# Kernel tuning notes

Hardware: AMD Instinct MI355X
Metric: run time of the kernel (lower is better)

## Reference

```python
import jax, jax.numpy as jnp
import numpy as np

BOX = 5  # box_size (odd)
PATTERN_SCALE = 16.0


def setup_inputs() -> dict:
    key = jax.random.key(0)
    k1, k2 = jax.random.split(key)
    x = jax.random.normal(k1, (1, 1, 480, 640), dtype=jnp.float32)
    # buffer: uniform in [-pattern_scale, pattern_scale], shape [num_pairs, 2, 2]
    pair_offsets = (jax.random.uniform(k2, (256, 2, 2), dtype=jnp.float32) - 0.5) * 2.0 * PATTERN_SCALE
    return {"x": x, "pair_offsets": pair_offsets}


def _box_average(x, box):
    # replicate-pad then stride-1 average pool => same-size box average
    pad = box // 2
    xp = jnp.pad(x, ((0, 0), (0, 0), (pad, pad), (pad, pad)), mode='edge')
    s = jax.lax.reduce_window(xp, 0.0, jax.lax.add,
                              (1, 1, box, box), (1, 1, 1, 1), 'VALID')
    return s / float(box * box)


def _grid_sample_offsets(img_flat, offsets, B, H, W):
    """Bilinear grid_sample with border padding, align_corners=True,
    for per-pair translational grids. img_flat: [B, H*W]; offsets: [P, 2] (dy, dx).
    Returns [B, P, H, W]."""
    scale_y = 2.0 / (H - 1 + 1e-8)
    scale_x = 2.0 / (W - 1 + 1e-8)
    base_y = jnp.linspace(-1.0, 1.0, H, dtype=img_flat.dtype)[None, :, None]  # [1,H,1]
    base_x = jnp.linspace(-1.0, 1.0, W, dtype=img_flat.dtype)[None, None, :]  # [1,1,W]
    gy = base_y + offsets[:, 0, None, None] * scale_y  # [P,H,1]
    gx = base_x + offsets[:, 1, None, None] * scale_x  # [P,1,W]
    # unnormalize (align_corners=True) and clip coords (padding_mode='border')
    py = jnp.clip((gy + 1.0) * 0.5 * (H - 1), 0.0, H - 1.0)  # [P,H,1]
    px = jnp.clip((gx + 1.0) * 0.5 * (W - 1), 0.0, W - 1.0)  # [P,1,W]
    y0 = jnp.floor(py)
    x0 = jnp.floor(px)
    wy = py - y0  # [P,H,1]
    wx = px - x0  # [P,1,W]
    y0i = y0.astype(jnp.int32)
    x0i = x0.astype(jnp.int32)
    y1i = jnp.minimum(y0i + 1, H - 1)
    x1i = jnp.minimum(x0i + 1, W - 1)

    def gather(yi, xi):
        idx = yi * W + xi  # broadcast -> [P,H,W]
        return jnp.take(img_flat, idx, axis=1)  # [B,P,H,W]

    v = (gather(y0i, x0i) * (1.0 - wy) * (1.0 - wx)
         + gather(y0i, x1i) * (1.0 - wy) * wx
         + gather(y1i, x0i) * wy * (1.0 - wx)
         + gather(y1i, x1i) * wy * wx)
    return v


def reference(x, pair_offsets):
    B, C, H, W = x.shape
    box_avg = _box_average(x, BOX)            # [B,1,H,W]
    img_flat = box_avg[:, 0].reshape(B, H * W)
    s1 = _grid_sample_offsets(img_flat, pair_offsets[:, 0, :], B, H, W)
    s2 = _grid_sample_offsets(img_flat, pair_offsets[:, 1, :], B, H, W)
    return s1 - s2  # binarize=False -> raw differences, [B, P, H, W]
```

## Files before the change

kernel.cpp:

```cpp
#include <hip/hip_runtime.h>

#define H 480
#define W 640
#define NP 256
#define HW (H * W)

#define P1_BLK 16
#define P2_BLK 9
#define P3_BLK 120

#define P1_TOTAL (NP * P1_BLK)
#define P2_TOTAL (NP * (P1_BLK + P2_BLK))
#define TOTAL_BLK (NP * (P1_BLK + P2_BLK + P3_BLK))

__global__ __launch_bounds__(256) void box_avg_kernel(const float* __restrict__ x,
                                                      float* __restrict__ box) {
    int idx = blockIdx.x * 256 + threadIdx.x;
    int i = idx / W;
    int j = idx - i * W;
    float s = 0.f;
#pragma unroll
    for (int dy = -2; dy <= 2; ++dy) {
        int yy = min(max(i + dy, 0), H - 1);
        const float* row = x + yy * W;
#pragma unroll
        for (int dx = -2; dx <= 2; ++dx) {
            int xx = min(max(j + dx, 0), W - 1);
            s += row[xx];
        }
    }
    box[idx] = s * 0.04f;
}

template<int S>
__device__ __forceinline__ void hlerp8(const float4 P, const float4 Q, const float4 R,
                                       float wx, float h[8]) {
    const float c[12] = {P.x, P.y, P.z, P.w, Q.x, Q.y, Q.z, Q.w, R.x, R.y, R.z, R.w};
#pragma unroll
    for (int k = 0; k < 8; ++k)
        h[k] = fmaf(wx, c[S + k + 1] - c[S + k], c[S + k]);
}

#define DISPATCH_H(sv, ...)                              \
    switch (sv) {                                        \
        case 0:  hlerp8<0>(__VA_ARGS__); break;          \
        case 1:  hlerp8<1>(__VA_ARGS__); break;          \
        case 2:  hlerp8<2>(__VA_ARGS__); break;          \
        default: hlerp8<3>(__VA_ARGS__); break;          \
    }

__global__ __launch_bounds__(256) void bad_desc_kernel(const float* __restrict__ box,
                                                       const float* __restrict__ po,
                                                       float* __restrict__ out) {
    int b = blockIdx.x;
    if (b < P1_TOTAL) {
        int p = b >> 4;
        int t = ((b - (p << 4)) << 8) + threadIdx.x;
        int band = t / 72;
        if (band >= 56) return;
        int g = t - band * 72;
        int i0 = 16 + (band << 3);
        int j  = 32 + (g << 3);

        float dy1 = po[p * 4 + 0];
        float dx1 = po[p * 4 + 1];
        float dy2 = po[p * 4 + 2];
        float dx2 = po[p * 4 + 3];

        float fj = (float)j;

        float xf1 = fj + dx1;
        float fl1 = floorf(xf1);
        int   x01 = (int)fl1;
        float wx1 = xf1 - fl1;
        int   s1  = __builtin_amdgcn_readfirstlane(x01 & 3);
        int   m1  = min(max(x01 - (x01 & 3), 0), W - 12);

        float xf2 = fj + dx2;
        float fl2 = floorf(xf2);
        int   x02 = (int)fl2;
        float wx2 = xf2 - fl2;
        int   s2  = __builtin_amdgcn_readfirstlane(x02 & 3);
        int   m2  = min(max(x02 - (x02 & 3), 0), W - 12);

        float fdy1 = floorf(dy1);
        float wy1  = dy1 - fdy1;
        int   rA   = min(max(i0 + (int)fdy1, 0), H - 9);
        float fdy2 = floorf(dy2);
        float wy2  = dy2 - fdy2;
        int   rB   = min(max(i0 + (int)fdy2, 0), H - 9);

        const float* baseA = box + rA * W + m1;
        const float* baseB = box + rB * W + m2;

        float h1p[8], h2p[8], h1c[8], h2c[8];
        {
            const float4* ra = (const float4*)baseA;
            const float4* rb = (const float4*)baseB;
            float4 Pa = ra[0], Qa = ra[1], Ra = ra[2];
            float4 Pb = rb[0], Qb = rb[1], Rb = rb[2];
            DISPATCH_H(s1, Pa, Qa, Ra, wx1, h1p);
            DISPATCH_H(s2, Pb, Qb, Rb, wx2, h2p);
        }

        float* o = out + ((size_t)p * HW + (size_t)i0 * W + (size_t)j);
        for (int k = 1; k <= 8; ++k) {
            const float4* ra = (const float4*)(baseA + k * W);
            const float4* rb = (const float4*)(baseB + k * W);
            float4 Pa = ra[0], Qa = ra[1], Ra = ra[2];
            float4 Pb = rb[0], Qb = rb[1], Rb = rb[2];
            DISPATCH_H(s1, Pa, Qa, Ra, wx1, h1c);
            DISPATCH_H(s2, Pb, Qb, Rb, wx2, h2c);

            float v[8];
#pragma unroll
            for (int q = 0; q < 8; ++q) {
                float a = fmaf(wy1, h1c[q] - h1p[q], h1p[q]);
                float c = fmaf(wy2, h2c[q] - h2p[q], h2p[q]);
                v[q] = a - c;
                h1p[q] = h1c[q];
                h2p[q] = h2c[q];
            }
            float4 o0 = {v[0], v[1], v[2], v[3]};
            float4 o1 = {v[4], v[5], v[6], v[7]};
            *(float4*)(o)     = o0;
            *(float4*)(o + 4) = o1;
            o += W;
        }
    } else if (b < P2_TOTAL) {
        int b2 = b - P1_TOTAL;
        int p = b2 / P2_BLK;
        int t = (b2 - p * P2_BLK) * 256 + threadIdx.x;
        int ii = t / 72;
        int g  = t - ii * 72;
        int i  = (ii < 16) ? ii : 448 + ii;
        int j  = 32 + (g << 3);

        float dy1 = po[p * 4 + 0];
        float dx1 = po[p * 4 + 1];
        float dy2 = po[p * 4 + 2];
        float dx2 = po[p * 4 + 3];

        float fi = (float)i;
        float fj = (float)j;

        float py1 = fminf(fmaxf(fi + dy1, 0.f), (float)(H - 1));
        int   ya0 = (int)py1;
        float wy1 = py1 - (float)ya0;
        int   ya1 = min(ya0 + 1, H - 1);

        float xf1 = fj + dx1;
        float fl1 = floorf(xf1);
        int   x01 = (int)fl1;
        float wx1 = xf1 - fl1;
        int   s1  = __builtin_amdgcn_readfirstlane(x01 & 3);
        int   m1  = min(max(x01 - (x01 & 3), 0), W - 12);

        const float4* r1a = (const float4*)(box + ya0 * W + m1);
        const float4* r1b = (const float4*)(box + ya1 * W + m1);
        float4 Pa = r1a[0], Qa = r1a[1], Ra = r1a[2];
        float4 Pb = r1b[0], Qb = r1b[1], Rb = r1b[2];
        float ha[8], hb[8];
        DISPATCH_H(s1, Pa, Qa, Ra, wx1, ha);
        DISPATCH_H(s1, Pb, Qb, Rb, wx1, hb);

        float py2 = fminf(fmaxf(fi + dy2, 0.f), (float)(H - 1));
        int   yb0 = (int)py2;
        float wy2 = py2 - (float)yb0;
        int   yb1 = min(yb0 + 1, H - 1);

        float xf2 = fj + dx2;
        float fl2 = floorf(xf2);
        int   x02 = (int)fl2;
        float wx2 = xf2 - fl2;
        int   s2  = __builtin_amdgcn_readfirstlane(x02 & 3);
        int   m2  = min(max(x02 - (x02 & 3), 0), W - 12);

        const float4* r2a = (const float4*)(box + yb0 * W + m2);
        const float4* r2b = (const float4*)(box + yb1 * W + m2);
        float4 Pc = r2a[0], Qc = r2a[1], Rc = r2a[2];
        float4 Pd = r2b[0], Qd = r2b[1], Rd = r2b[2];
        float hc[8], hd[8];
        DISPATCH_H(s2, Pc, Qc, Rc, wx2, hc);
        DISPATCH_H(s2, Pd, Qd, Rd, wx2, hd);

        float v[8];
#pragma unroll
        for (int q = 0; q < 8; ++q) {
            float a = fmaf(wy1, hb[q] - ha[q], ha[q]);
            float c = fmaf(wy2, hd[q] - hc[q], hc[q]);
            v[q] = a - c;
        }
        float* o = out + ((size_t)p * HW + (size_t)i * W + (size_t)j);
        float4 o0 = {v[0], v[1], v[2], v[3]};
        float4 o1 = {v[4], v[5], v[6], v[7]};
        *(float4*)(o)     = o0;
        *(float4*)(o + 4) = o1;
    } else {
        int b2 = b - P2_TOTAL;
        int p = b2 / P3_BLK;
        int t = (b2 - p * P3_BLK) * 256 + threadIdx.x;
        int i = t >> 6;
        int c = t & 63;
        int j = (c < 32) ? c : 576 + c;

        float dy1 = po[p * 4 + 0];
        float dx1 = po[p * 4 + 1];
        float dy2 = po[p * 4 + 2];
        float dx2 = po[p * 4 + 3];

        float fi = (float)i;
        float fj = (float)j;

        float py1 = fminf(fmaxf(fi + dy1, 0.f), (float)(H - 1));
        int   ya0 = (int)py1;
        float wy1 = py1 - (float)ya0;
        int   ya1 = min(ya0 + 1, H - 1);
        const float* r1a = box + ya0 * W;
        const float* r1b = box + ya1 * W;

        float px = fminf(fmaxf(fj + dx1, 0.f), (float)(W - 1));
        int   x0 = (int)px;
        float wx = px - (float)x0;
        int   x1 = min(x0 + 1, W - 1);
        float a0 = r1a[x0], a1 = r1a[x1];
        float b0 = r1b[x0], b1 = r1b[x1];
        float h0 = fmaf(wx, a1 - a0, a0);
        float h1 = fmaf(wx, b1 - b0, b0);
        float v1 = fmaf(wy1, h1 - h0, h0);

        float py2 = fminf(fmaxf(fi + dy2, 0.f), (float)(H - 1));
        int   yb0 = (int)py2;
        float wy2 = py2 - (float)yb0;
        int   yb1 = min(yb0 + 1, H - 1);
        const float* r2a = box + yb0 * W;
        const float* r2b = box + yb1 * W;

        float qx = fminf(fmaxf(fj + dx2, 0.f), (float)(W - 1));
        int   u0 = (int)qx;
        float ux = qx - (float)u0;
        int   u1 = min(u0 + 1, W - 1);
        float c0 = r2a[u0], c1 = r2a[u1];
        float d0 = r2b[u0], d1 = r2b[u1];
        float g0 = fmaf(ux, c1 - c0, c0);
        float g1 = fmaf(ux, d1 - d0, d0);
        float v2 = fmaf(wy2, g1 - g0, g0);

        out[(size_t)p * HW + (size_t)i * W + (size_t)j] = v1 - v2;
    }
}

extern "C" void kernel_launch(void* const* d_in, const int* in_sizes, int n_in,
                              void* d_out, int out_size, void* d_ws, size_t ws_size,
                              hipStream_t stream) {
    const float* x  = (const float*)d_in[0];
    const float* po = (const float*)d_in[1];
    float* out = (float*)d_out;
    float* box = (float*)d_ws;

    box_avg_kernel<<<HW / 256, 256, 0, stream>>>(x, box);
    bad_desc_kernel<<<TOTAL_BLK, 256, 0, stream>>>(box, po, out);
}
```

Before: 342.7 us.

## Use nontemporal output stores and band-process left/right edge columns with row reuse

All output writes become nontemporal stores so the large write-once output stream does not pollute cache. The left/right edge-column region, which used one pixel per thread, is split into an interior band path and a top/bottom remainder path. In the band path each thread walks 8 rows and reuses the previous row's horizontal interpolation, which cuts gather loads roughly in half. The band path relies on the clamp being inactive in interior rows, using the floor of the offset plus a clamped base row.

Result: faster. 331.5 us (-3.3%).

```diff
diff --git a/kernel.cpp b/kernel.cpp
--- a/kernel.cpp
+++ b/kernel.cpp
@@ -7,11 +7,20 @@
 
 #define P1_BLK 16
 #define P2_BLK 9
-#define P3_BLK 120
+#define P3_BLK 14
+#define P4_BLK 8
 
 #define P1_TOTAL (NP * P1_BLK)
 #define P2_TOTAL (NP * (P1_BLK + P2_BLK))
-#define TOTAL_BLK (NP * (P1_BLK + P2_BLK + P3_BLK))
+#define P3_TOTAL (NP * (P1_BLK + P2_BLK + P3_BLK))
+#define TOTAL_BLK (NP * (P1_BLK + P2_BLK + P3_BLK + P4_BLK))
+
+typedef float f32x4 __attribute__((ext_vector_type(4)));
+
+__device__ __forceinline__ void nt_store4(float* p, float a, float b, float c, float d) {
+    f32x4 v = {a, b, c, d};
+    __builtin_nontemporal_store(v, (f32x4*)p);
+}
 
 __global__ __launch_bounds__(256) void box_avg_kernel(const float* __restrict__ x,
                                                       float* __restrict__ box) {
@@ -121,10 +130,8 @@
                 h1p[q] = h1c[q];
                 h2p[q] = h2c[q];
             }
-            float4 o0 = {v[0], v[1], v[2], v[3]};
-            float4 o1 = {v[4], v[5], v[6], v[7]};
-            *(float4*)(o)     = o0;
-            *(float4*)(o + 4) = o1;
+            nt_store4(o,     v[0], v[1], v[2], v[3]);
+            nt_store4(o + 4, v[4], v[5], v[6], v[7]);
             o += W;
         }
     } else if (b < P2_TOTAL) {
@@ -192,16 +199,72 @@
             v[q] = a - c;
         }
         float* o = out + ((size_t)p * HW + (size_t)i * W + (size_t)j);
-        float4 o0 = {v[0], v[1], v[2], v[3]};
-        float4 o1 = {v[4], v[5], v[6], v[7]};
-        *(float4*)(o)     = o0;
-        *(float4*)(o + 4) = o1;
-    } else {
+        nt_store4(o,     v[0], v[1], v[2], v[3]);
+        nt_store4(o + 4, v[4], v[5], v[6], v[7]);
+    } else if (b < P3_TOTAL) {
         int b2 = b - P2_TOTAL;
         int p = b2 / P3_BLK;
         int t = (b2 - p * P3_BLK) * 256 + threadIdx.x;
-        int i = t >> 6;
+        int band = t >> 6;
         int c = t & 63;
+        int i0 = 16 + (band << 3);
+        int j  = (c < 32) ? c : 576 + c;
+
+        float dy1 = po[p * 4 + 0];
+        float dx1 = po[p * 4 + 1];
+        float dy2 = po[p * 4 + 2];
+        float dx2 = po[p * 4 + 3];
+
+        float fj = (float)j;
+
+        float px1 = fminf(fmaxf(fj + dx1, 0.f), (float)(W - 1));
+        int   xa0 = (int)px1;
+        float wxa = px1 - (float)xa0;
+        int   xa1 = min(xa0 + 1, W - 1);
+
+        float px2 = fminf(fmaxf(fj + dx2, 0.f), (float)(W - 1));
+        int   xb0 = (int)px2;
+        float wxb = px2 - (float)xb0;
+        int   xb1 = min(xb0 + 1, W - 1);
+
+        float fdy1 = floorf(dy1);
+        float wy1  = dy1 - fdy1;
+        int   rA   = min(max(i0 + (int)fdy1, 0), H - 9);
+        float fdy2 = floorf(dy2);
+        float wy2  = dy2 - fdy2;
+        int   rB   = min(max(i0 + (int)fdy2, 0), H - 9);
+
+        const float* pA = box + rA * W;
+        const float* pB = box + rB * W;
+
+        float a0 = pA[xa0], a1 = pA[xa1];
+        float h1p = fmaf(wxa, a1 - a0, a0);
+        float b0 = pB[xb0], b1 = pB[xb1];
+        float h2p = fmaf(wxb, b1 - b0, b0);
+
+        float* o = out + ((size_t)p * HW + (size_t)i0 * W + (size_t)j);
+        for (int k = 1; k <= 8; ++k) {
+            const float* qA = pA + k * W;
+            const float* qB = pB + k * W;
+            float c0 = qA[xa0], c1 = qA[xa1];
+            float h1c = fmaf(wxa, c1 - c0, c0);
+            float d0 = qB[xb0], d1 = qB[xb1];
+            float h2c = fmaf(wxb, d1 - d0, d0);
+
+            float va = fmaf(wy1, h1c - h1p, h1p);
+            float vb = fmaf(wy2, h2c - h2p, h2p);
+            __builtin_nontemporal_store(va - vb, o);
+            h1p = h1c;
+            h2p = h2c;
+            o += W;
+        }
+    } else {
+        int b2 = b - P3_TOTAL;
+        int p = b2 >> 3;
+        int t = ((b2 - (p << 3)) << 8) + threadIdx.x;
+        int ii = t >> 6;
+        int c = t & 63;
+        int i = (ii < 16) ? ii : 448 + ii;
         int j = (c < 32) ? c : 576 + c;
 
         float dy1 = po[p * 4 + 0];
@@ -246,7 +309,7 @@
         float g1 = fmaf(ux, d1 - d0, d0);
         float v2 = fmaf(wy2, g1 - g0, g0);
 
-        out[(size_t)p * HW + (size_t)i * W + (size_t)j] = v1 - v2;
+        __builtin_nontemporal_store(v1 - v2, out + ((size_t)p * HW + (size_t)i * W + (size_t)j));
     }
 }
 
```
